# Kernel optimization log

Hardware: AMD Instinct MI355X
Metric: run time of the kernel (lower is better)

Reference implementation:

```python
import jax, jax.numpy as jnp
from jax import lax
import numpy as np
import math

B, N, M, SIG, HID, NFEAT, OUT, H = 256, 512, 16, 256, 256, 3, 10, 256
ALPHA, BETA = 1.0, 0.5


def setup_inputs() -> dict:
    key = jax.random.key(0)
    ks = jax.random.split(key, 12)
    s_g = 1.0 / math.sqrt(HID)
    s_f = 1.0 / math.sqrt(SIG)
    return {
        "x": jax.random.normal(ks[0], (B, 1, H, H), jnp.float32),
        "unif": jax.random.uniform(ks[1], (B, N), jnp.float32),
        "z": jax.random.normal(ks[2], (B, N, 2), jnp.float32),
        "m_g_params": jax.random.normal(ks[3], (1, 6 * M), jnp.float32),
        "gc1_w": jax.random.uniform(ks[4], (NFEAT, HID), jnp.float32, -s_g, s_g),
        "gc1_b": jax.random.uniform(ks[5], (HID,), jnp.float32, -s_g, s_g),
        "gc2_w": jax.random.uniform(ks[6], (HID, HID), jnp.float32, -s_g, s_g),
        "gc2_b": jax.random.uniform(ks[7], (HID,), jnp.float32, -s_g, s_g),
        "collapser1": 0.1 * jax.random.normal(ks[8], (SIG, N), jnp.float32),
        "collapser2": 0.1 * jax.random.normal(ks[9], (SIG, N), jnp.float32),
        "fcf_w": jax.random.uniform(ks[10], (OUT, SIG), jnp.float32, -s_f, s_f),
        "fcf_b": jax.random.uniform(ks[11], (OUT,), jnp.float32, -s_f, s_f),
    }


def _mixture_fields(m_g_params):
    # torch: split [num_sample, 6M] into M chunks of 6, stack -> [M, N, 6],
    # split along last dim, then .view(N, M) in C-order on the [M, N] field.
    raw = m_g_params.reshape(M, 6)  # [M, 6]
    return [jnp.broadcast_to(raw[:, j][:, None], (M, N)).reshape(N, M) for j in range(6)]


def reference(x, unif, z, m_g_params, gc1_w, gc1_b, gc2_w, gc2_b,
              collapser1, collapser2, fcf_w, fcf_b):
    pi_f, mux_f, muy_f, sx_f, sy_f, rho_f = _mixture_fields(m_g_params)
    pi = jax.nn.softmax(pi_f, axis=-1)            # [N, M]
    # categorical sampling via CDF inversion, vectorized over batch
    cdf = jnp.cumsum(pi, axis=-1)                 # [N, M]
    idx = jnp.argmax(unif[:, :, None] < cdf[None], axis=-1)  # [B, N]
    row = jnp.arange(N)[None, :]
    gat = lambda f: f[row, idx]                   # [B, N]
    mux, muy = gat(mux_f), gat(muy_f)
    sx, sy = jnp.exp(gat(sx_f)), jnp.exp(gat(sy_f))
    rho = jnp.tanh(gat(rho_f))
    # reparameterized bivariate-normal sample via Cholesky (lower)
    z1, z2 = z[..., 0], z[..., 1]
    xs = mux + sx * z1
    ys = muy + sy * (rho * z1 + jnp.sqrt(1.0 - rho * rho) * z2)
    # torch MVN.sample() is no_grad -> detach samples
    xs_c, ys_c = lax.stop_gradient(xs), lax.stop_gradient(ys)
    dx, dy = xs_c - mux, ys_c - muy
    omr2 = 1.0 - rho * rho
    quad = (dx * dx / (sx * sx) - 2.0 * rho * dx * dy / (sx * sy) + dy * dy / (sy * sy)) / omr2
    logprob = (-jnp.log(2.0 * jnp.pi) - jnp.log(sx * sy)
               - 0.5 * jnp.log(omr2) - 0.5 * quad)  # [B, N]
    full_log_prob = logprob.sum(axis=-1)           # [B]
    loc = jnp.tanh(jnp.stack([xs_c, ys_c], axis=-1))  # [B, N, 2]
    # adjacency: inverse shifted pairwise squared distance
    diff = loc[:, :, None, :] - loc[:, None, :, :]  # [B, N, N, 2]
    adj = 1.0 / (ALPHA + BETA * jnp.sum(diff * diff, axis=-1))  # [B, N, N]
    # pixel gather: denormalize (trunc toward zero, like torch .long())
    pix = jnp.trunc(0.5 * (loc + 1.0) * H - 0.1).astype(jnp.int32)
    pix = jnp.clip(pix, 0, H - 1)
    bidx = jnp.arange(B)[:, None]
    pv = x[bidx, :, pix[..., 0], pix[..., 1]]      # [B, N, 1]
    feat = jnp.concatenate([pv, loc], axis=-1)     # [B, N, 3]
    # GCN (eval mode: no dropout)
    s1 = jax.nn.relu(jnp.einsum('bnm,bmh->bnh', adj, feat @ gc1_w) + gc1_b)
    s2 = jax.nn.relu(jnp.einsum('bnm,bmh->bnh', adj, s1 @ gc2_w) + gc2_b)
    # nn.Softmax() (no dim) on 3D input resolves to dim=0 in torch
    g1 = jax.nn.softmax(jnp.einsum('sn,bnh->bsh', collapser1, s1), axis=0)
    g2 = jax.nn.softmax(jnp.einsum('sn,bnh->bsh', collapser2, s2), axis=0)
    sig = (g1 + g2).sum(axis=2)                    # [B, SIG]
    out = jax.nn.softmax(sig @ fcf_w.T + fcf_b, axis=-1)  # [B, OUT]
    return out, full_log_prob
```

## Files before the change

kernel.cpp:

```cpp
#include <hip/hip_runtime.h>
#include <hip/hip_bf16.h>
#include <math.h>

#define Bx   256
#define Nx   512
#define SIGx 256
#define HIDx 256
#define OUTx 10
#define Hx   256

typedef __attribute__((ext_vector_type(4))) float f32x4;
typedef __attribute__((ext_vector_type(2))) uint uint2v;
typedef long fp8x8;
typedef unsigned char uchar;

#define WAITVM(N) asm volatile("s_waitcnt vmcnt(" #N ")" ::: "memory")
#define MEMFENCE() asm volatile("" ::: "memory")

__device__ inline uchar f2fp8(float v) {
    int r = __builtin_amdgcn_cvt_pk_fp8_f32(v, 0.0f, 0, false);
    return (uchar)(r & 0xff);
}
__device__ inline uint pk4fp8(float a0, float a1, float a2, float a3) {
    int r = __builtin_amdgcn_cvt_pk_fp8_f32(a0, a1, 0, false);
    r = __builtin_amdgcn_cvt_pk_fp8_f32(a2, a3, r, true);
    return (uint)r;
}

__device__ inline void gload_lds16(const uchar* g, uchar* l) {
    __builtin_amdgcn_global_load_lds(
        (const __attribute__((address_space(1))) uint*)g,
        (__attribute__((address_space(3))) uint*)l, 16, 0, 0);
}
__device__ inline const uchar* laddr(const uchar* base, int row, int kb) {
    int ps = (kb >> 4) ^ ((row >> 1) & 3) ^ ((row >> 4) & 3);
    return base + row*64 + ps*16 + (kb & 15);
}

__global__ __launch_bounds__(512) void kA_sample(
    const float* __restrict__ x, const float* __restrict__ z,
    const float* __restrict__ mg, float* __restrict__ feat,
    float* __restrict__ flp)
{
    int b = blockIdx.x;
    int n = threadIdx.x;
    int g = n >> 5;
    float mux = mg[g*6+1];
    float muy = mg[g*6+2];
    float sxv = expf(mg[g*6+3]);
    float syv = expf(mg[g*6+4]);
    float rho = tanhf(mg[g*6+5]);
    float z1 = z[((size_t)b*Nx + n)*2 + 0];
    float z2 = z[((size_t)b*Nx + n)*2 + 1];
    float omr2 = 1.0f - rho*rho;
    float xs = mux + sxv*z1;
    float ys = muy + syv*(rho*z1 + sqrtf(omr2)*z2);
    float dx = xs - mux, dy = ys - muy;
    float quad = (dx*dx/(sxv*sxv) - 2.0f*rho*dx*dy/(sxv*syv) + dy*dy/(syv*syv)) / omr2;
    float logprob = -1.8378770664093453f - logf(sxv*syv) - 0.5f*logf(omr2) - 0.5f*quad;
    float lx = tanhf(xs), ly = tanhf(ys);
    int px = (int)truncf(0.5f*(lx+1.0f)*(float)Hx - 0.1f);
    int py = (int)truncf(0.5f*(ly+1.0f)*(float)Hx - 0.1f);
    px = px < 0 ? 0 : (px > Hx-1 ? Hx-1 : px);
    py = py < 0 ? 0 : (py > Hx-1 ? Hx-1 : py);
    float pv = x[(size_t)b*Hx*Hx + (size_t)px*Hx + py];
    size_t fo = ((size_t)b*Nx + n)*3;
    feat[fo+0] = pv; feat[fo+1] = lx; feat[fo+2] = ly;

    __shared__ float red[512];
    red[n] = logprob;
    __syncthreads();
    for (int st = 256; st > 0; st >>= 1) {
        if (n < st) red[n] += red[n+st];
        __syncthreads();
    }
    if (n == 0) flp[b] = red[0];
}

__global__ __launch_bounds__(256) void kPrep(
    const float* __restrict__ c1, const float* __restrict__ c2,
    const float* __restrict__ w2,
    uchar* __restrict__ c1q, uchar* __restrict__ c2q, uchar* __restrict__ w2tq)
{
    int idx = blockIdx.x*256 + threadIdx.x;
    if (idx < SIGx*Nx) {
        c1q[idx] = f2fp8(16.0f * c1[idx]);
        c2q[idx] = f2fp8(16.0f * c2[idx]);
    }
    if (idx < HIDx*HIDx) {
        int i = idx >> 8, j = idx & 255;
        w2tq[idx] = f2fp8(16.0f * w2[j*HIDx + i]);
    }
}

__global__ __launch_bounds__(512) void kFuse1(
    const float* __restrict__ featL, const float* __restrict__ w1,
    const float* __restrict__ b1,
    uchar* __restrict__ adjAll, uchar* __restrict__ s1tAll)
{
    int b = blockIdx.x;
    const float* fb = featL + (size_t)b*Nx*3;
    uchar* adj = adjAll + (size_t)b*Nx*Nx;
    uchar* s1t = s1tAll + (size_t)b*HIDx*Nx;

    __shared__ float fpv[Nx], flx[Nx], fly[Nx], fH[Nx];
    __shared__ float w1s[3*HIDx], b1s[HIDx];
    __shared__ float Gp[4][3][Nx];

    int t = threadIdx.x;
    {
        float pv = fb[t*3+0], lx = fb[t*3+1], ly = fb[t*3+2];
        fpv[t] = pv; flx[t] = lx; fly[t] = ly;
        fH[t] = fmaf(0.5f*lx, lx, fmaf(0.5f*ly, ly, 1.0f));
    }
    for (int i = t; i < 3*HIDx; i += 512) w1s[i] = w1[i];
    if (t < HIDx) b1s[t] = b1[t];
    __syncthreads();

    int tq = t & 127;
    int mc = t >> 7;
    int n4 = tq*4;

    float xn[4], yn[4], cn[4];
    #pragma unroll
    for (int e = 0; e < 4; ++e) {
        xn[e] = flx[n4+e]; yn[e] = fly[n4+e];
        cn[e] = fmaf(0.5f*xn[e], xn[e], 0.5f*yn[e]*yn[e]);
    }
    float G0[4] = {}, G1[4] = {}, G2[4] = {};

    int m0 = mc*128;
    #pragma unroll 4
    for (int mm = 0; mm < 128; ++mm) {
        int m = m0 + mm;
        float hx = fH[m], fx = flx[m], fy = fly[m];
        float a[4];
        #pragma unroll
        for (int e = 0; e < 4; ++e) {
            float s = fmaf(-yn[e], fy, fmaf(-xn[e], fx, hx + cn[e]));
            a[e] = __builtin_amdgcn_rcpf(s);
            G0[e] = fmaf(a[e], fpv[m], G0[e]);
            G1[e] = fmaf(a[e], fx, G1[e]);
            G2[e] = fmaf(a[e], fy, G2[e]);
        }
        *(uint*)(adj + (size_t)m*Nx + n4) = pk4fp8(a[0], a[1], a[2], a[3]);
    }

    *(f32x4*)&Gp[mc][0][n4] = (f32x4){G0[0],G0[1],G0[2],G0[3]};
    *(f32x4*)&Gp[mc][1][n4] = (f32x4){G1[0],G1[1],G1[2],G1[3]};
    *(f32x4*)&Gp[mc][2][n4] = (f32x4){G2[0],G2[1],G2[2],G2[3]};
    __syncthreads();

    f32x4 T0 = {}, T1 = {}, T2 = {};
    #pragma unroll
    for (int j = 0; j < 4; ++j) {
        T0 += *(const f32x4*)&Gp[j][0][n4];
        T1 += *(const f32x4*)&Gp[j][1][n4];
        T2 += *(const f32x4*)&Gp[j][2][n4];
    }

    int hc = mc;
    #pragma unroll 4
    for (int hh = 0; hh < 64; ++hh) {
        int h = hc*64 + hh;
        float w0 = w1s[h], wA = w1s[HIDx+h], wB = w1s[2*HIDx+h], bb = b1s[h];
        float v0 = fminf(fmaxf(fmaf(T0.x,w0, fmaf(T1.x,wA, fmaf(T2.x,wB, bb))), 0.0f), 448.0f);
        float v1 = fminf(fmaxf(fmaf(T0.y,w0, fmaf(T1.y,wA, fmaf(T2.y,wB, bb))), 0.0f), 448.0f);
        float v2 = fminf(fmaxf(fmaf(T0.z,w0, fmaf(T1.z,wA, fmaf(T2.z,wB, bb))), 0.0f), 448.0f);
        float v3 = fminf(fmaxf(fmaf(T0.w,w0, fmaf(T1.w,wA, fmaf(T2.w,wB, bb))), 0.0f), 448.0f);
        *(uint*)(s1t + (size_t)h*Nx + n4) = pk4fp8(v0, v1, v2, v3);
    }
}

__global__ __launch_bounds__(512, 4) void kGemmAdj8(
    const uchar* __restrict__ Aall, const uchar* __restrict__ adjAll,
    const float* __restrict__ bias, uchar* __restrict__ outAll)
{
    int b    = blockIdx.x;
    int tile = blockIdx.y;
    int rt = tile >> 2;
    int ct = tile & 3;
    const uchar* A = Aall + (size_t)b*HIDx*Nx;
    const uchar* Badj = adjAll + (size_t)b*Nx*Nx;
    uchar* outp = outAll + (size_t)b*HIDx*Nx;

    __shared__ __align__(16) uchar Als[2][128*64];
    __shared__ __align__(16) uchar Bls[2][128*64];
    int t = threadIdx.x;
    int lane = t & 63, wave = t >> 6;
    int wr = wave >> 2, wc = wave & 3;
    int q = lane >> 4, c16 = lane & 15;
    int r0 = rt*128, n0 = ct*128;
    int srow = wave*16 + (lane >> 2);
    int pu   = lane & 3;
    int sl   = pu ^ ((srow>>1)&3) ^ ((srow>>4)&3);
    f32x4 acc[4][2] = {};

    auto stage = [&](int buf, int kkv) {
        gload_lds16(A + (size_t)(r0+srow)*Nx + kkv + sl*16, Als[buf] + wave*1024);
        gload_lds16(Badj + (size_t)(n0+srow)*Nx + kkv + sl*16, Bls[buf] + wave*1024);
    };

    const int nt = Nx/64;
    stage(0, 0);
    for (int i = 0; i < nt; ++i) {
        if (i < nt-1) { stage((i+1)&1, (i+1)*64); WAITVM(2); }
        else WAITVM(0);
        __builtin_amdgcn_s_barrier();
        MEMFENCE();
        const uchar* Ac = Als[i&1];
        const uchar* Bc = Bls[i&1];
        #pragma unroll
        for (int ks = 0; ks < 64; ks += 32) {
            fp8x8 af[4], bfr[2];
            #pragma unroll
            for (int i2 = 0; i2 < 4; ++i2)
                af[i2] = *(const fp8x8*)laddr(Ac, wr*64 + i2*16 + c16, ks + q*8);
            #pragma unroll
            for (int j = 0; j < 2; ++j)
                bfr[j] = *(const fp8x8*)laddr(Bc, wc*32 + j*16 + c16, ks + q*8);
            #pragma unroll
            for (int i2 = 0; i2 < 4; ++i2)
                #pragma unroll
                for (int j = 0; j < 2; ++j)
                    acc[i2][j] = __builtin_amdgcn_mfma_f32_16x16x32_fp8_fp8(af[i2], bfr[j], acc[i2][j], 0, 0, 0);
        }
        MEMFENCE();
        __builtin_amdgcn_s_barrier();
        MEMFENCE();
    }
    #pragma unroll
    for (int i = 0; i < 4; ++i) {
        int rowb = r0 + wr*64 + i*16 + q*4;
        #pragma unroll
        for (int j = 0; j < 2; ++j) {
            int col = n0 + wc*32 + j*16 + c16;
            #pragma unroll
            for (int r = 0; r < 4; ++r) {
                float v = fmaxf(acc[i][j][r] + bias[rowb + r], 0.0f) * 0.25f;
                outp[(size_t)(rowb + r)*Nx + col] = f2fp8(fminf(v, 448.0f));
            }
        }
    }
}

__global__ __launch_bounds__(512, 4) void kGstd8(
    const uchar* __restrict__ Ash, const uchar* __restrict__ Ball,
    uchar* __restrict__ outAll, float oscale)
{
    int b    = blockIdx.x;
    int tile = blockIdx.y;
    int rt = tile >> 1;
    int ct = tile & 1;
    const uchar* B = Ball + (size_t)b*HIDx*Nx;
    uchar* outp = outAll + (size_t)b*HIDx*256;

    __shared__ __align__(16) uchar Als[2][128*64];
    __shared__ __align__(16) uchar Bls[2][128*64];
    int t = threadIdx.x;
    int lane = t & 63, wave = t >> 6;
    int wr = wave >> 2, wc = wave & 3;
    int q = lane >> 4, c16 = lane & 15;
    int r0 = rt*128, n0 = ct*128;
    int srow = wave*16 + (lane >> 2);
    int pu   = lane & 3;
    int sl   = pu ^ ((srow>>1)&3) ^ ((srow>>4)&3);
    f32x4 acc[4][2] = {};

    auto stage = [&](int buf, int kkv) {
        gload_lds16(Ash + (size_t)(r0+srow)*Nx + kkv + sl*16, Als[buf] + wave*1024);
        gload_lds16(B + (size_t)(n0+srow)*Nx + kkv + sl*16, Bls[buf] + wave*1024);
    };

    const int nt = Nx/64;
    stage(0, 0);
    for (int i = 0; i < nt; ++i) {
        if (i < nt-1) { stage((i+1)&1, (i+1)*64); WAITVM(2); }
        else WAITVM(0);
        __builtin_amdgcn_s_barrier();
        MEMFENCE();
        const uchar* Ac = Als[i&1];
        const uchar* Bc = Bls[i&1];
        #pragma unroll
        for (int ks = 0; ks < 64; ks += 32) {
            fp8x8 af[4], bfr[2];
            #pragma unroll
            for (int i2 = 0; i2 < 4; ++i2)
                af[i2] = *(const fp8x8*)laddr(Ac, wr*64 + i2*16 + c16, ks + q*8);
            #pragma unroll
            for (int j = 0; j < 2; ++j)
                bfr[j] = *(const fp8x8*)laddr(Bc, wc*32 + j*16 + c16, ks + q*8);
            #pragma unroll
            for (int i2 = 0; i2 < 4; ++i2)
                #pragma unroll
                for (int j = 0; j < 2; ++j)
                    acc[i2][j] = __builtin_amdgcn_mfma_f32_16x16x32_fp8_fp8(af[i2], bfr[j], acc[i2][j], 0, 0, 0);
        }
        MEMFENCE();
        __builtin_amdgcn_s_barrier();
        MEMFENCE();
    }
    #pragma unroll
    for (int i = 0; i < 4; ++i) {
        int rowb = r0 + wr*64 + i*16 + q*4;
        #pragma unroll
        for (int j = 0; j < 2; ++j) {
            int col = n0 + wc*32 + j*16 + c16;
            #pragma unroll
            for (int r = 0; r < 4; ++r) {
                float v = acc[i][j][r] * oscale;
                v = fminf(fmaxf(v, -448.0f), 448.0f);
                outp[(size_t)(rowb + r)*256 + col] = f2fp8(v);
            }
        }
    }
}

__global__ __launch_bounds__(512, 4) void kGstdT8(
    const uchar* __restrict__ Ash, const uchar* __restrict__ Ball,
    uchar* __restrict__ outAll, float oscale)
{
    const int K = 256, NC = 512;
    int b    = blockIdx.x;
    int tile = blockIdx.y;
    int rt = tile >> 2;
    int ct = tile & 3;
    const uchar* B = Ball + (size_t)b*HIDx*Nx;
    uchar* outp = outAll + (size_t)b*HIDx*NC;

    __shared__ __align__(16) uchar Als[2][128*64];
    __shared__ __align__(16) uchar Bls[2][128*64];
    int t = threadIdx.x;
    int lane = t & 63, wave = t >> 6;
    int wr = wave >> 2, wc = wave & 3;
    int q = lane >> 4, c16 = lane & 15;
    int r0 = rt*128, n0 = ct*128;
    int srow = wave*16 + (lane >> 2);
    int pu   = lane & 3;
    int sl   = pu ^ ((srow>>1)&3) ^ ((srow>>4)&3);
    int pi  = t & 31;
    int g   = t >> 5;
    int nc8 = g & 7;
    int ch  = g >> 3;
    f32x4 acc[4][2] = {};

    auto stageA = [&](int buf, int kkv) {
        gload_lds16(Ash + (size_t)(r0+srow)*K + kkv + sl*16, Als[buf] + wave*1024);
    };
    auto loadBT = [&](int kkv, uint2v& v0, uint2v& v1) {
        int hk = kkv + 2*pi;
        const uchar* g0 = B + (size_t)hk*NC + n0 + nc8*16 + ch*8;
        v0 = *(const uint2v*)g0;
        v1 = *(const uint2v*)(g0 + NC);
    };
    auto writeBT = [&](int buf, const uint2v& v0, const uint2v& v1) {
        const uchar* pa = (const uchar*)&v0;
        const uchar* qa = (const uchar*)&v1;
        int kb = 2*pi;
        int s  = kb >> 4;
        #pragma unroll
        for (int e = 0; e < 8; ++e) {
            int row = nc8*16 + ch*8 + e;
            int ps = s ^ ((row>>1)&3) ^ ((row>>4)&3);
            *(ushort*)(Bls[buf] + row*64 + ps*16 + (kb & 15)) =
                (ushort)pa[e] | ((ushort)qa[e] << 8);
        }
    };
    auto mfmaStep = [&](int buf) {
        const uchar* Ac = Als[buf];
        const uchar* Bc = Bls[buf];
        #pragma unroll
        for (int ks = 0; ks < 64; ks += 32) {
            fp8x8 af[4], bfr[2];
            #pragma unroll
            for (int i = 0; i < 4; ++i)
                af[i] = *(const fp8x8*)laddr(Ac, wr*64 + i*16 + c16, ks + q*8);
            #pragma unroll
            for (int j = 0; j < 2; ++j)
                bfr[j] = *(const fp8x8*)laddr(Bc, wc*32 + j*16 + c16, ks + q*8);
            #pragma unroll
            for (int i = 0; i < 4; ++i)
                #pragma unroll
                for (int j = 0; j < 2; ++j)
                    acc[i][j] = __builtin_amdgcn_mfma_f32_16x16x32_fp8_fp8(af[i], bfr[j], acc[i][j], 0, 0, 0);
        }
    };

    uint2v bv0, bv1;
    stageA(0, 0);
    loadBT(0, bv0, bv1); writeBT(0, bv0, bv1);
    __syncthreads();
    for (int kk = 0; kk < K; kk += 64) {
        int cur = (kk >> 6) & 1, nxt = cur ^ 1;
        bool more = (kk + 64) < K;
        if (more) {
            stageA(nxt, kk + 64);
            loadBT(kk + 64, bv0, bv1);
        }
        mfmaStep(cur);
        if (more) writeBT(nxt, bv0, bv1);
        __syncthreads();
    }
    #pragma unroll
    for (int i = 0; i < 4; ++i) {
        int rowb = r0 + wr*64 + i*16 + q*4;
        #pragma unroll
        for (int j = 0; j < 2; ++j) {
            int col = n0 + wc*32 + j*16 + c16;
            #pragma unroll
            for (int r = 0; r < 4; ++r) {
                float v = acc[i][j][r] * oscale;
                v = fminf(fmaxf(v, -448.0f), 448.0f);
                outp[(size_t)(rowb + r)*NC + col] = f2fp8(v);
            }
        }
    }
}

__global__ __launch_bounds__(512) void kF1q(
    const uchar* __restrict__ t1, const uchar* __restrict__ t2,
    float* __restrict__ m1, float* __restrict__ rd1,
    float* __restrict__ m2, float* __restrict__ rd2)
{
    int s = blockIdx.x;
    int t = threadIdx.x;
    int hq = t & 63;
    int bq = t >> 6;
    const size_t str = (size_t)SIGx*HIDx;
    size_t base = (size_t)(bq*32)*str + (size_t)s*HIDx + hq*4;

    float mv1[4], dv1[4], mv2[4], dv2[4];
    #pragma unroll
    for (int e = 0; e < 4; ++e) { mv1[e]=-3.0e38f; dv1[e]=0.0f; mv2[e]=-3.0e38f; dv2[e]=0.0f; }

    for (int i = 0; i < 32; ++i) {
        uint u1 = *(const uint*)(t1 + base + (size_t)i*str);
        uint u2 = *(const uint*)(t2 + base + (size_t)i*str);
        float v1[4], v2[4];
        v1[0] = __builtin_amdgcn_cvt_f32_fp8(u1, 0);
        v1[1] = __builtin_amdgcn_cvt_f32_fp8(u1, 1);
        v1[2] = __builtin_amdgcn_cvt_f32_fp8(u1, 2);
        v1[3] = __builtin_amdgcn_cvt_f32_fp8(u1, 3);
        v2[0] = __builtin_amdgcn_cvt_f32_fp8(u2, 0);
        v2[1] = __builtin_amdgcn_cvt_f32_fp8(u2, 1);
        v2[2] = __builtin_amdgcn_cvt_f32_fp8(u2, 2);
        v2[3] = __builtin_amdgcn_cvt_f32_fp8(u2, 3);
        #pragma unroll
        for (int e = 0; e < 4; ++e) {
            float mn;
            mn = fmaxf(mv1[e], v1[e]);
            dv1[e] = dv1[e]*__expf(mv1[e]-mn) + __expf(v1[e]-mn); mv1[e] = mn;
            mn = fmaxf(mv2[e], v2[e]);
            dv2[e] = dv2[e]*__expf(mv2[e]-mn) + __expf(v2[e]-mn); mv2[e] = mn;
        }
    }

    __shared__ float pm1[8][256], pd1[8][256], pm2[8][256], pd2[8][256];
    #pragma unroll
    for (int e = 0; e < 4; ++e) {
        pm1[bq][hq*4+e] = mv1[e]; pd1[bq][hq*4+e] = dv1[e];
        pm2[bq][hq*4+e] = mv2[e]; pd2[bq][hq*4+e] = dv2[e];
    }
    __syncthreads();

    if (t < 256) {
        int h = t;
        float m = -3.0e38f, d = 0.0f;
        #pragma unroll
        for (int j = 0; j < 8; ++j) {
            float mm = pm1[j][h], dd = pd1[j][h];
            float mn = fmaxf(m, mm);
            d = d*__expf(m-mn) + dd*__expf(mm-mn);
            m = mn;
        }
        size_t o = (size_t)s*HIDx + h;
        m1[o] = m; rd1[o] = 1.0f/d;
    } else {
        int h = t - 256;
        float m = -3.0e38f, d = 0.0f;
        #pragma unroll
        for (int j = 0; j < 8; ++j) {
            float mm = pm2[j][h], dd = pd2[j][h];
            float mn = fmaxf(m, mm);
            d = d*__expf(m-mn) + dd*__expf(mm-mn);
            m = mn;
        }
        size_t o = (size_t)s*HIDx + h;
        m2[o] = m; rd2[o] = 1.0f/d;
    }
}

__global__ __launch_bounds__(256) void kF2q(
    const uchar* __restrict__ t1, const uchar* __restrict__ t2,
    const float* __restrict__ m1, const float* __restrict__ rd1,
    const float* __restrict__ m2, const float* __restrict__ rd2,
    float* __restrict__ sig)
{
    int b = blockIdx.y;
    int sq = threadIdx.x >> 6;
    int s = blockIdx.x*4 + sq;
    int hq = threadIdx.x & 63;
    size_t sh = (size_t)s*HIDx + hq*4;
    size_t tb = ((size_t)b*SIGx + s)*HIDx + hq*4;
    uint u1 = *(const uint*)(t1 + tb);
    uint u2 = *(const uint*)(t2 + tb);
    f32x4 a1 = *(const f32x4*)&m1[sh];
    f32x4 r1 = *(const f32x4*)&rd1[sh];
    f32x4 a2 = *(const f32x4*)&m2[sh];
    f32x4 r2 = *(const f32x4*)&rd2[sh];
    float v = 0.0f;
    v += __expf(__builtin_amdgcn_cvt_f32_fp8(u1,0) - a1.x) * r1.x;
    v += __expf(__builtin_amdgcn_cvt_f32_fp8(u1,1) - a1.y) * r1.y;
    v += __expf(__builtin_amdgcn_cvt_f32_fp8(u1,2) - a1.z) * r1.z;
    v += __expf(__builtin_amdgcn_cvt_f32_fp8(u1,3) - a1.w) * r1.w;
    v += __expf(__builtin_amdgcn_cvt_f32_fp8(u2,0) - a2.x) * r2.x;
    v += __expf(__builtin_amdgcn_cvt_f32_fp8(u2,1) - a2.y) * r2.y;
    v += __expf(__builtin_amdgcn_cvt_f32_fp8(u2,2) - a2.z) * r2.z;
    v += __expf(__builtin_amdgcn_cvt_f32_fp8(u2,3) - a2.w) * r2.w;

    __shared__ float red[256];
    red[threadIdx.x] = v;
    __syncthreads();
    for (int st = 32; st > 0; st >>= 1) {
        if (hq < st) red[threadIdx.x] += red[threadIdx.x + st];
        __syncthreads();
    }
    if (hq == 0) sig[(size_t)b*SIGx + s] = red[sq*64];
}

__global__ __launch_bounds__(256) void kG_out(
    const float* __restrict__ sig, const float* __restrict__ fw,
    const float* __restrict__ fb, float* __restrict__ out)
{
    int b = blockIdx.x;
    int tid = threadIdx.x;
    __shared__ float red[256];
    __shared__ float logits[OUTx];
    float sv = sig[(size_t)b*SIGx + tid];
    for (int o = 0; o < OUTx; ++o) {
        red[tid] = sv * fw[o*SIGx + tid];
        __syncthreads();
        for (int st = 128; st > 0; st >>= 1) {
            if (tid < st) red[tid] += red[tid+st];
            __syncthreads();
        }
        if (tid == 0) logits[o] = red[0] + fb[o];
        __syncthreads();
    }
    if (tid == 0) {
        float mx = logits[0];
        for (int o = 1; o < OUTx; ++o) mx = fmaxf(mx, logits[o]);
        float dd = 0.0f; float e[OUTx];
        for (int o = 0; o < OUTx; ++o) { e[o] = expf(logits[o]-mx); dd += e[o]; }
        float inv = 1.0f/dd;
        for (int o = 0; o < OUTx; ++o) out[(size_t)b*OUTx + o] = e[o]*inv;
    }
}

static inline size_t alignup(size_t b) { return (b + 255) & ~(size_t)255; }

extern "C" void kernel_launch(void* const* d_in, const int* in_sizes, int n_in,
                              void* d_out, int out_size, void* d_ws, size_t ws_size,
                              hipStream_t stream)
{
    const float* x   = (const float*)d_in[0];
    const float* z   = (const float*)d_in[2];
    const float* mg  = (const float*)d_in[3];
    const float* w1  = (const float*)d_in[4];
    const float* b1  = (const float*)d_in[5];
    const float* w2  = (const float*)d_in[6];
    const float* b2  = (const float*)d_in[7];
    const float* c1  = (const float*)d_in[8];
    const float* c2  = (const float*)d_in[9];
    const float* fw  = (const float*)d_in[10];
    const float* fbv = (const float*)d_in[11];
    float* out = (float*)d_out;
    float* flp = out + (size_t)Bx*OUTx;
    (void)in_sizes; (void)n_in; (void)out_size;

    char* ws = (char*)d_ws;
    size_t off = 0;
    auto alloc = [&](size_t bytes) -> char* {
        char* p = ws + off; off += alignup(bytes); return p;
    };
    float*  feat = (float*)alloc((size_t)Bx*Nx*3*4);
    uchar*  c1q  = (uchar*)alloc((size_t)SIGx*Nx);
    uchar*  c2q  = (uchar*)alloc((size_t)SIGx*Nx);
    uchar*  w2tq = (uchar*)alloc((size_t)HIDx*HIDx);
    uchar*  t1   = (uchar*)alloc((size_t)Bx*SIGx*HIDx);
    uchar*  t2   = (uchar*)alloc((size_t)Bx*SIGx*HIDx);
    float*  m1   = (float*)alloc((size_t)SIGx*HIDx*4);
    float*  d1   = (float*)alloc((size_t)SIGx*HIDx*4);
    float*  m2   = (float*)alloc((size_t)SIGx*HIDx*4);
    float*  d2   = (float*)alloc((size_t)SIGx*HIDx*4);
    float*  sig  = (float*)alloc((size_t)Bx*SIGx*4);
    size_t fixed = off;

    int BC = 1;
    for (int c = Bx; c >= 1; c >>= 1) {
        size_t need = fixed + alignup((size_t)c*Nx*Nx)
                            + 2*alignup((size_t)c*HIDx*Nx);
        if (need <= ws_size) { BC = c; break; }
    }
    uchar* Padj = (uchar*)alloc((size_t)BC*Nx*Nx);
    uchar* P1   = (uchar*)alloc((size_t)BC*HIDx*Nx);
    uchar* P2   = (uchar*)alloc((size_t)BC*HIDx*Nx);

    hipLaunchKernelGGL(kA_sample, dim3(Bx), dim3(Nx), 0, stream, x, z, mg, feat, flp);
    hipLaunchKernelGGL(kPrep, dim3(512), dim3(256), 0, stream, c1, c2, w2, c1q, c2q, w2tq);

    const int nch = Bx / BC;
    for (int c = 0; c < nch; ++c) {
        int b0 = c * BC;
        const float* featL = feat + (size_t)b0*Nx*3;
        uchar* t1L = t1 + (size_t)b0*SIGx*HIDx;
        uchar* t2L = t2 + (size_t)b0*SIGx*HIDx;
        hipLaunchKernelGGL(kFuse1, dim3(BC), dim3(512), 0, stream,
                           featL, w1, b1, Padj, P2);
        hipLaunchKernelGGL(kGstd8, dim3(BC, 4), dim3(512), 0, stream,
                           c1q, P2, t1L, 0.0625f);
        hipLaunchKernelGGL(kGstdT8, dim3(BC, 8), dim3(512), 0, stream,
                           w2tq, P2, P1, 0.0625f);
        hipLaunchKernelGGL(kGemmAdj8, dim3(BC, 8), dim3(512), 0, stream, P1, Padj, b2, P2);
        hipLaunchKernelGGL(kGstd8, dim3(BC, 4), dim3(512), 0, stream,
                           c2q, P2, t2L, 0.25f);
    }

    hipLaunchKernelGGL(kF1q, dim3(SIGx), dim3(512), 0, stream,
                       t1, t2, m1, d1, m2, d2);
    hipLaunchKernelGGL(kF2q, dim3(SIGx/4, Bx), dim3(256), 0, stream,
                       t1, t2, m1, d1, m2, d2, sig);
    hipLaunchKernelGGL(kG_out, dim3(Bx), dim3(256), 0, stream, sig, fw, fbv, out);
}
```

Measured before the change: 288.4 us.

## Split adjacency/GCN-layer1 kernel across two column blocks and batch output reductions

kFuse1 is split into two blocks per batch, each handling 256 output columns with 8 warps-groups over 64 rows each, doubling the grid to raise occupancy and shorten per-block serial loops. The final output kernel now reduces all 10 logits in a single shared-memory tree instead of ten sequential reductions, cutting barrier count. The split duplicates the small shared-memory staging of features per block.

```diff
diff --git a/kernel.cpp b/kernel.cpp
--- a/kernel.cpp
+++ b/kernel.cpp
@@ -93,19 +93,20 @@
     }
 }
 
-__global__ __launch_bounds__(512) void kFuse1(
+__global__ __launch_bounds__(512) void kFuse1S(
     const float* __restrict__ featL, const float* __restrict__ w1,
     const float* __restrict__ b1,
     uchar* __restrict__ adjAll, uchar* __restrict__ s1tAll)
 {
     int b = blockIdx.x;
+    int n0 = blockIdx.y * 256;
     const float* fb = featL + (size_t)b*Nx*3;
     uchar* adj = adjAll + (size_t)b*Nx*Nx;
     uchar* s1t = s1tAll + (size_t)b*HIDx*Nx;
 
     __shared__ float fpv[Nx], flx[Nx], fly[Nx], fH[Nx];
     __shared__ float w1s[3*HIDx], b1s[HIDx];
-    __shared__ float Gp[4][3][Nx];
+    __shared__ float Gp[8][3][256];
 
     int t = threadIdx.x;
     {
@@ -117,9 +118,10 @@
     if (t < HIDx) b1s[t] = b1[t];
     __syncthreads();
 
-    int tq = t & 127;
-    int mc = t >> 7;
-    int n4 = tq*4;
+    int tq = t & 63;
+    int mc = t >> 6;
+    int lc = tq*4;
+    int n4 = n0 + lc;
 
     float xn[4], yn[4], cn[4];
     #pragma unroll
@@ -129,9 +131,9 @@
     }
     float G0[4] = {}, G1[4] = {}, G2[4] = {};
 
-    int m0 = mc*128;
+    int m0 = mc*64;
     #pragma unroll 4
-    for (int mm = 0; mm < 128; ++mm) {
+    for (int mm = 0; mm < 64; ++mm) {
         int m = m0 + mm;
         float hx = fH[m], fx = flx[m], fy = fly[m];
         float a[4];
@@ -146,23 +148,23 @@
         *(uint*)(adj + (size_t)m*Nx + n4) = pk4fp8(a[0], a[1], a[2], a[3]);
     }
 
-    *(f32x4*)&Gp[mc][0][n4] = (f32x4){G0[0],G0[1],G0[2],G0[3]};
-    *(f32x4*)&Gp[mc][1][n4] = (f32x4){G1[0],G1[1],G1[2],G1[3]};
-    *(f32x4*)&Gp[mc][2][n4] = (f32x4){G2[0],G2[1],G2[2],G2[3]};
+    *(f32x4*)&Gp[mc][0][lc] = (f32x4){G0[0],G0[1],G0[2],G0[3]};
+    *(f32x4*)&Gp[mc][1][lc] = (f32x4){G1[0],G1[1],G1[2],G1[3]};
+    *(f32x4*)&Gp[mc][2][lc] = (f32x4){G2[0],G2[1],G2[2],G2[3]};
     __syncthreads();
 
     f32x4 T0 = {}, T1 = {}, T2 = {};
     #pragma unroll
-    for (int j = 0; j < 4; ++j) {
-        T0 += *(const f32x4*)&Gp[j][0][n4];
-        T1 += *(const f32x4*)&Gp[j][1][n4];
-        T2 += *(const f32x4*)&Gp[j][2][n4];
+    for (int j = 0; j < 8; ++j) {
+        T0 += *(const f32x4*)&Gp[j][0][lc];
+        T1 += *(const f32x4*)&Gp[j][1][lc];
+        T2 += *(const f32x4*)&Gp[j][2][lc];
     }
 
     int hc = mc;
     #pragma unroll 4
-    for (int hh = 0; hh < 64; ++hh) {
-        int h = hc*64 + hh;
+    for (int hh = 0; hh < 32; ++hh) {
+        int h = hc*32 + hh;
         float w0 = w1s[h], wA = w1s[HIDx+h], wB = w1s[2*HIDx+h], bb = b1s[h];
         float v0 = fminf(fmaxf(fmaf(T0.x,w0, fmaf(T1.x,wA, fmaf(T2.x,wB, bb))), 0.0f), 448.0f);
         float v1 = fminf(fmaxf(fmaf(T0.y,w0, fmaf(T1.y,wA, fmaf(T2.y,wB, bb))), 0.0f), 448.0f);
@@ -534,25 +536,33 @@
 {
     int b = blockIdx.x;
     int tid = threadIdx.x;
-    __shared__ float red[256];
-    __shared__ float logits[OUTx];
+    __shared__ float red[OUTx][257];
     float sv = sig[(size_t)b*SIGx + tid];
-    for (int o = 0; o < OUTx; ++o) {
-        red[tid] = sv * fw[o*SIGx + tid];
+    #pragma unroll
+    for (int o = 0; o < OUTx; ++o)
+        red[o][tid] = sv * fw[o*SIGx + tid];
+    __syncthreads();
+    for (int st = 128; st > 0; st >>= 1) {
+        if (tid < st) {
+            #pragma unroll
+            for (int o = 0; o < OUTx; ++o)
+                red[o][tid] += red[o][tid + st];
+        }
         __syncthreads();
-        for (int st = 128; st > 0; st >>= 1) {
-            if (tid < st) red[tid] += red[tid+st];
-            __syncthreads();
-        }
-        if (tid == 0) logits[o] = red[0] + fb[o];
-        __syncthreads();
     }
     if (tid == 0) {
-        float mx = logits[0];
-        for (int o = 1; o < OUTx; ++o) mx = fmaxf(mx, logits[o]);
+        float logits[OUTx];
+        float mx = -3.0e38f;
+        #pragma unroll
+        for (int o = 0; o < OUTx; ++o) {
+            logits[o] = red[o][0] + fb[o];
+            mx = fmaxf(mx, logits[o]);
+        }
         float dd = 0.0f; float e[OUTx];
+        #pragma unroll
         for (int o = 0; o < OUTx; ++o) { e[o] = expf(logits[o]-mx); dd += e[o]; }
         float inv = 1.0f/dd;
+        #pragma unroll
         for (int o = 0; o < OUTx; ++o) out[(size_t)b*OUTx + o] = e[o]*inv;
     }
 }
@@ -615,7 +625,7 @@
         const float* featL = feat + (size_t)b0*Nx*3;
         uchar* t1L = t1 + (size_t)b0*SIGx*HIDx;
         uchar* t2L = t2 + (size_t)b0*SIGx*HIDx;
-        hipLaunchKernelGGL(kFuse1, dim3(BC), dim3(512), 0, stream,
+        hipLaunchKernelGGL(kFuse1S, dim3(BC, 2), dim3(512), 0, stream,
                            featL, w1, b1, Padj, P2);
         hipLaunchKernelGGL(kGstd8, dim3(BC, 4), dim3(512), 0, stream,
                            c1q, P2, t1L, 0.0625f);
```

Result: faster. 279.1 us (-3.2%).
